# Performance work log

Hardware: AMD Instinct MI355X
Metric: run time of the kernel (lower is better)

The kernel has to match this reference:

```python
import jax, jax.numpy as jnp
import numpy as np

D_MODEL = 512
N = 1024
BS = 64


def setup_inputs() -> dict:
    key = jax.random.key(0)
    ks = jax.random.split(key, 4)
    x = jax.random.normal(ks[0], (BS, N, D_MODEL), dtype=jnp.float32)
    # nn.Linear init per init_weights(): weight ~ N(0, 0.001), bias = 0
    Wq = 0.001 * jax.random.normal(ks[1], (D_MODEL, D_MODEL), dtype=jnp.float32)
    Wk = 0.001 * jax.random.normal(ks[2], (D_MODEL, D_MODEL), dtype=jnp.float32)
    Wv = 0.001 * jax.random.normal(ks[3], (D_MODEL, D_MODEL), dtype=jnp.float32)
    bq = jnp.zeros((D_MODEL,), dtype=jnp.float32)
    bk = jnp.zeros((D_MODEL,), dtype=jnp.float32)
    bv = jnp.zeros((D_MODEL,), dtype=jnp.float32)
    pos_bias = jnp.ones((N, N), dtype=jnp.float32)  # nn.Parameter(ones)
    return {"x": x, "Wq": Wq, "bq": bq, "Wk": Wk, "bk": bk,
            "Wv": Wv, "bv": bv, "pos_bias": pos_bias}


def reference(x, Wq, bq, Wk, bk, Wv, bv, pos_bias):
    # q,k,v: [bs, n, d] via Linear (y = x W^T + b)
    q = jnp.einsum('bnd,ed->bne', x, Wq) + bq
    k = jnp.einsum('bnd,ed->bne', x, Wk) + bk
    v = jnp.einsum('bnd,ed->bne', x, Wv) + bv
    # exp(k[b,j,d] + bias[i,j]) factorizes exactly: exp(bias) * exp(k).
    # This avoids the (n, bs, n, d) broadcast intermediate of the original
    # while computing identical math.
    ek = jnp.exp(k)                                   # [bs, n, d]
    eb = jnp.exp(pos_bias)                            # [n_i, n_j]
    numerator = jnp.einsum('ij,bjd->bid', eb, ek * v)  # sum over j
    denominator = jnp.einsum('ij,bjd->bid', eb, ek)
    out = jax.nn.sigmoid(q) * (numerator / denominator)  # [bs, n, d]
    return out
```

## Files before the change

kernel.cpp:

```cpp
#include <hip/hip_runtime.h>
#include <hip/hip_bf16.h>
#include <stdint.h>


#define NSEQ 1024
#define DM   512

typedef __attribute__((ext_vector_type(8))) short bf16x8;
typedef __attribute__((ext_vector_type(4))) float f32x4;

static __device__ __forceinline__ float b2f(unsigned short u) {
    union { uint32_t i; float f; } c; c.i = ((uint32_t)u) << 16; return c.f;
}
static __device__ __forceinline__ unsigned short f2b(float f) {
    union { float f; uint32_t i; } c; c.f = f;
    uint32_t r = c.i + 0x7FFFu + ((c.i >> 16) & 1u);
    return (unsigned short)(r >> 16);
}
static __device__ __forceinline__ void gl_lds16(const unsigned short* g, unsigned short* l) {
    __builtin_amdgcn_global_load_lds(
        (const __attribute__((address_space(1))) unsigned int*)(g),
        (__attribute__((address_space(3))) unsigned int*)(l), 16, 0, 0);
}

#define PH_BAR() do { asm volatile("" ::: "memory"); \
    __builtin_amdgcn_s_barrier(); asm volatile("" ::: "memory"); } while (0)

__global__ void k_flag0(unsigned int* flag) { *flag = 0u; }

__global__ void k_flag(const float* __restrict__ pb, unsigned int* __restrict__ flag) {
    int i = blockIdx.x * 256 + threadIdx.x;
    float4 v = reinterpret_cast<const float4*>(pb)[i];
    float p0 = pb[0];
    if (v.x != p0 || v.y != p0 || v.z != p0 || v.w != p0) atomicOr(flag, 1u);
}

__global__ void k_eb(const float* __restrict__ pb, unsigned short* __restrict__ eb,
                     const unsigned int* __restrict__ flag) {
    if (*flag == 0u) return;
    int i = blockIdx.x * 256 + threadIdx.x;
    float4 v = reinterpret_cast<const float4*>(pb)[i];
    union { unsigned short u[4]; uint2 p; } o;
    o.u[0] = f2b(__expf(v.x)); o.u[1] = f2b(__expf(v.y));
    o.u[2] = f2b(__expf(v.z)); o.u[3] = f2b(__expf(v.w));
    reinterpret_cast<uint2*>(eb)[i] = o.p;
}

__global__ void k_cvt(const float* __restrict__ src, unsigned short* __restrict__ dst) {
    int i = blockIdx.x * 256 + threadIdx.x;
    const float4* p = reinterpret_cast<const float4*>(src) + (size_t)i * 2;
    float4 f0 = p[0], f1 = p[1];
    union { unsigned short u[8]; int4 v; } o;
    o.u[0]=f2b(f0.x); o.u[1]=f2b(f0.y); o.u[2]=f2b(f0.z); o.u[3]=f2b(f0.w);
    o.u[4]=f2b(f1.x); o.u[5]=f2b(f1.y); o.u[6]=f2b(f1.z); o.u[7]=f2b(f1.w);
    reinterpret_cast<int4*>(dst)[i] = o.v;
}

__global__ void k_cvt_kv(const float* __restrict__ src, unsigned short* __restrict__ Wb,
                         int toff) {
    int i = blockIdx.x * 256 + threadIdx.x;
    int r = i >> 6, c8 = i & 63;
    const float4* p = reinterpret_cast<const float4*>(src + (size_t)r * DM + c8 * 8);
    float4 f0 = p[0], f1 = p[1];
    union { unsigned short u[8]; int4 v; } o;
    o.u[0]=f2b(f0.x); o.u[1]=f2b(f0.y); o.u[2]=f2b(f0.z); o.u[3]=f2b(f0.w);
    o.u[4]=f2b(f1.x); o.u[5]=f2b(f1.y); o.u[6]=f2b(f1.z); o.u[7]=f2b(f1.w);
    int r2 = 512 + ((r >> 7) << 8) + ((r & 127) << 1) + toff;
    *reinterpret_cast<int4*>(&Wb[(size_t)r2 * DM + c8 * 8]) = o.v;
}

__launch_bounds__(512)
__global__ void k_kv(const float* __restrict__ x,
                     const unsigned short* __restrict__ Wb,
                     const float* __restrict__ bk, const float* __restrict__ bv,
                     unsigned short* __restrict__ Z,
                     float* __restrict__ P,
                     const unsigned int* __restrict__ flag)
{
    extern __shared__ unsigned short smem[];
    const int bid = blockIdx.x;
    const int logical = (bid & 7) * 128 + (bid >> 3);
    const int mtile = logical >> 2, e4 = logical & 3;
    const int brow = mtile * 256;
    const int b = brow >> 10, jtile = (brow >> 8) & 3;
    const bool uni = (*flag == 0u);

    const int tid = threadIdx.x;
    const int lane = tid & 63, wave = tid >> 6;
    const int wr = wave >> 2, wq = wave & 3;
    const int lrow = lane & 15, lkg = lane >> 4;
    const int po = lane >> 3, sub0 = (lane >> 2) & 1, qp = lane & 3;

    const float* Ax = x + (size_t)brow * DM;
    const unsigned short* Bb = Wb + (size_t)(512 + e4 * 256) * DM;

    f32x4 acc[8][4];
    const f32x4 z4 = {0.f, 0.f, 0.f, 0.f};
    #pragma unroll
    for (int a = 0; a < 8; ++a)
        #pragma unroll
        for (int c = 0; c < 4; ++c) acc[a][c] = z4;

    auto stgB = [&](int s, int h, int t) {
        int p = h * 64 + wave * 8 + po;
        int r = p * 2 + sub0;
        int col = (t << 5) + ((qp ^ (p & 3)) << 3);
        gl_lds16(Bb + (size_t)r * DM + col,
                 smem + 16384 + s * 8192 + (h * 64 + wave * 8) * 64);
    };
    auto ldAreg = [&](int t, int h, float4* f) {
        int p = h * 64 + wave * 8 + po;
        int r = p * 2 + sub0;
        int col = (t << 5) + ((qp ^ (p & 3)) << 3);
        const float4* sp = reinterpret_cast<const float4*>(Ax + (size_t)r * DM + col);
        f[0] = sp[0]; f[1] = sp[1];
    };
    auto wrA = [&](int s, int h, const float4* f) {
        union { unsigned short u[8]; int4 v; } o;
        o.u[0]=f2b(f[0].x); o.u[1]=f2b(f[0].y); o.u[2]=f2b(f[0].z); o.u[3]=f2b(f[0].w);
        o.u[4]=f2b(f[1].x); o.u[5]=f2b(f[1].y); o.u[6]=f2b(f[1].z); o.u[7]=f2b(f[1].w);
        *reinterpret_cast<int4*>(
            smem + s * 8192 + (h * 64 + wave * 8) * 64 + lane * 8) = o.v;
    };
    auto ldAf = [&](int s, int h, bf16x8* af) {
        const unsigned short* base = smem + s * 8192;
        #pragma unroll
        for (int mi = 0; mi < 4; ++mi) {
            int r = wr * 128 + h * 64 + mi * 16 + lrow, p = r >> 1;
            af[mi] = *reinterpret_cast<const bf16x8*>(
                base + p * 64 + (r & 1) * 32 + ((lkg ^ (p & 3)) << 3));
        }
    };
    auto ldBf = [&](int s, bf16x8* bf) {
        const unsigned short* base = smem + 16384 + s * 8192;
        #pragma unroll
        for (int ni = 0; ni < 4; ++ni) {
            int r = wq * 64 + ni * 16 + lrow, p = r >> 1;
            bf[ni] = *reinterpret_cast<const bf16x8*>(
                base + p * 64 + (r & 1) * 32 + ((lkg ^ (p & 3)) << 3));
        }
    };
    auto mfma16 = [&](int h, bf16x8* af, bf16x8* bf) {
        __builtin_amdgcn_s_setprio(1);
        #pragma unroll
        for (int mi = 0; mi < 4; ++mi)
            #pragma unroll
            for (int ni = 0; ni < 4; ++ni)
                acc[h * 4 + mi][ni] = __builtin_amdgcn_mfma_f32_16x16x32_bf16(
                    af[mi], bf[ni], acc[h * 4 + mi][ni], 0, 0, 0);
        __builtin_amdgcn_s_setprio(0);
    };

    {
        float4 fA0[2], fA1[2];
        ldAreg(0, 0, fA0); ldAreg(0, 1, fA1);
        stgB(0, 0, 0); stgB(0, 1, 0);
        wrA(0, 0, fA0); wrA(0, 1, fA1);
        __syncthreads();
    }
    #pragma unroll 1
    for (int t = 0; t < 16; ++t) {
        const int s = t & 1, sn = s ^ 1;
        const bool more = (t + 1 < 16);
        float4 fN0[2], fN1[2];
        if (more) {
            ldAreg(t + 1, 0, fN0); ldAreg(t + 1, 1, fN1);
            stgB(sn, 0, t + 1); stgB(sn, 1, t + 1);
        }
        bf16x8 af[4], bfr[4];
        ldBf(s, bfr); ldAf(s, 0, af);
        mfma16(0, af, bfr);
        ldAf(s, 1, af);
        mfma16(1, af, bfr);
        if (more) { wrA(sn, 0, fN0); wrA(sn, 1, fN1); }
        __syncthreads();
    }

    if (uni) {
        const int sub = lane & 1;
        float* SF = reinterpret_cast<float*>(smem);
        float se[4], sv2[4];
        #pragma unroll
        for (int ni = 0; ni < 4; ++ni) {
            int n = wq * 64 + ni * 16 + lrow;
            int d = e4 * 128 + (n >> 1);
            float bia = sub ? bv[d] : bk[d];
            float accv = 0.f, acce = 0.f;
            #pragma unroll
            for (int mi = 0; mi < 8; ++mi) {
                #pragma unroll
                for (int r = 0; r < 4; ++r) {
                    float val = acc[mi][ni][r] + bia;
                    float e = sub ? val : __expf(val);
                    float partner = __shfl_xor(e, 1);
                    if (!sub) { accv += e * partner; acce += e; }
                }
            }
            accv += __shfl_xor(accv, 16); accv += __shfl_xor(accv, 32);
            acce += __shfl_xor(acce, 16); acce += __shfl_xor(acce, 32);
            se[ni] = acce; sv2[ni] = accv;
        }
        __syncthreads();
        if (sub == 0 && lkg == 0) {
            #pragma unroll
            for (int ni = 0; ni < 4; ++ni) {
                int dl = wq * 32 + ni * 8 + (lrow >> 1);
                SF[wr * 256 + dl * 2]     = sv2[ni];
                SF[wr * 256 + dl * 2 + 1] = se[ni];
            }
        }
        __syncthreads();
        if (tid < 128) {
            int dl = tid, d = e4 * 128 + dl;
            float num = SF[dl * 2]     + SF[256 + dl * 2];
            float den = SF[dl * 2 + 1] + SF[256 + dl * 2 + 1];
            P[b * 2048 + jtile * 512 + d] = num;
            P[131072 + b * 2048 + jtile * 512 + d] = den;
        }
    } else {
        unsigned short* T = smem;
        #pragma unroll
        for (int pp = 0; pp < 2; ++pp) {
            __syncthreads();
            if (wr == pp) {
                #pragma unroll
                for (int mi = 0; mi < 8; ++mi) {
                    int m0 = mi*16 + lkg*4;
                    #pragma unroll
                    for (int ni = 0; ni < 4; ++ni) {
                        int n = wq*64 + ni*16 + lrow;
                        int sub = n & 1;
                        int d = e4 * 128 + (n >> 1);
                        float bia = sub ? bv[d] : bk[d];
                        union { unsigned short u[4]; uint2 p; } o;
                        #pragma unroll
                        for (int r = 0; r < 4; ++r) {
                            float tv = acc[mi][ni][r] + bia;
                            o.u[r] = f2b(sub ? tv : __expf(tv));
                        }
                        *reinterpret_cast<uint2*>(&T[n * 136 + m0]) = o.p;
                    }
                }
            }
            __syncthreads();
            const int j0 = (brow & (NSEQ - 1)) + pp * 128;
            #pragma unroll
            for (int it = 0; it < 8; ++it) {
                int idx = it * 512 + tid;
                int zr = idx >> 4, jg = idx & 15;
                int t = zr >> 7, dli = zr & 127;
                int d = e4 * 128 + dli;
                union { unsigned short u[8]; int4 v; } o;
                if (t == 0) {
                    union { unsigned short u[8]; int4 v; } pe, pv;
                    pe.v = *reinterpret_cast<const int4*>(&T[(2*dli)     * 136 + jg*8]);
                    pv.v = *reinterpret_cast<const int4*>(&T[(2*dli + 1) * 136 + jg*8]);
                    #pragma unroll
                    for (int j = 0; j < 8; ++j) o.u[j] = f2b(b2f(pe.u[j]) * b2f(pv.u[j]));
                } else {
                    o.v = *reinterpret_cast<const int4*>(&T[(2*dli) * 136 + jg*8]);
                }
                int nz = ((d >> 4) << 5) + t * 16 + (d & 15);
                size_t off = ((size_t)(b * NSEQ + nz)) * NSEQ + j0 + jg * 8;
                *reinterpret_cast<int4*>(&Z[off]) = o.v;
            }
        }
    }
}

__launch_bounds__(256)
__global__ void k_sum2(const float* __restrict__ P,
                       const unsigned int* __restrict__ flag,
                       float* __restrict__ R)
{
    if (*flag != 0u) return;
    int gid = blockIdx.x * 256 + threadIdx.x;
    int b = gid >> 9, d = gid & 511;
    const float* p0 = P + b * 2048 + d;
    const float* p1 = P + 131072 + b * 2048 + d;
    float num = p0[0] + p0[512] + p0[1024] + p0[1536];
    float den = p1[0] + p1[512] + p1[1024] + p1[1536];
    R[gid] = num / den;
}

__launch_bounds__(512)
__global__ void k_q(const float* __restrict__ x,
                    const unsigned short* __restrict__ Wb,
                    const float* __restrict__ bq,
                    const float* __restrict__ R,
                    unsigned short* __restrict__ s_out,
                    float* __restrict__ out,
                    const unsigned int* __restrict__ flag)
{
    extern __shared__ unsigned short smem[];
    const int bid = blockIdx.x;
    const int logical = (bid & 7) * 256 + (bid >> 3);
    const int mtile = logical >> 2, etile = logical & 3;
    const int brow = mtile * 128;
    const int ecol = etile * 128;
    const int b = brow >> 10;
    const bool uni = (*flag == 0u);

    const int tid = threadIdx.x;
    const int lane = tid & 63, wave = tid >> 6;
    const int wr = wave >> 2, wq = wave & 3;
    const int lrow = lane & 15, lkg = lane >> 4;
    const int po = lane >> 3, sub0 = (lane >> 2) & 1, qp = lane & 3;

    const float* Ax = x + (size_t)brow * DM;
    const unsigned short* Bb = Wb + (size_t)ecol * DM;

    f32x4 acc[4][2];
    const f32x4 z4 = {0.f, 0.f, 0.f, 0.f};
    #pragma unroll
    for (int a = 0; a < 4; ++a)
        #pragma unroll
        for (int c = 0; c < 2; ++c) acc[a][c] = z4;

    auto stgB = [&](int s, int t) {
        int p = wave * 8 + po;
        int r = p * 2 + sub0;
        int col = (t << 5) + ((qp ^ (p & 3)) << 3);
        gl_lds16(Bb + (size_t)r * DM + col,
                 smem + 8192 + s * 4096 + (wave * 8) * 64);
    };
    auto ldAreg = [&](int t, float4* f) {
        int p = wave * 8 + po;
        int r = p * 2 + sub0;
        int col = (t << 5) + ((qp ^ (p & 3)) << 3);
        const float4* sp = reinterpret_cast<const float4*>(Ax + (size_t)r * DM + col);
        f[0] = sp[0]; f[1] = sp[1];
    };
    auto wrA = [&](int s, const float4* f) {
        union { unsigned short u[8]; int4 v; } o;
        o.u[0]=f2b(f[0].x); o.u[1]=f2b(f[0].y); o.u[2]=f2b(f[0].z); o.u[3]=f2b(f[0].w);
        o.u[4]=f2b(f[1].x); o.u[5]=f2b(f[1].y); o.u[6]=f2b(f[1].z); o.u[7]=f2b(f[1].w);
        *reinterpret_cast<int4*>(
            smem + s * 4096 + (wave * 8) * 64 + lane * 8) = o.v;
    };
    auto ldAf = [&](int s, bf16x8* af) {
        const unsigned short* base = smem + s * 4096;
        #pragma unroll
        for (int mi = 0; mi < 4; ++mi) {
            int r = wr * 64 + mi * 16 + lrow, p = r >> 1;
            af[mi] = *reinterpret_cast<const bf16x8*>(
                base + p * 64 + (r & 1) * 32 + ((lkg ^ (p & 3)) << 3));
        }
    };
    auto ldBf = [&](int s, bf16x8* bf) {
        const unsigned short* base = smem + 8192 + s * 4096;
        #pragma unroll
        for (int ni = 0; ni < 2; ++ni) {
            int r = wq * 32 + ni * 16 + lrow, p = r >> 1;
            bf[ni] = *reinterpret_cast<const bf16x8*>(
                base + p * 64 + (r & 1) * 32 + ((lkg ^ (p & 3)) << 3));
        }
    };

    {
        float4 fA[2];
        ldAreg(0, fA);
        stgB(0, 0);
        wrA(0, fA);
        __syncthreads();
    }
    #pragma unroll 1
    for (int t = 0; t < 16; ++t) {
        const int s = t & 1, sn = s ^ 1;
        const bool more = (t + 1 < 16);
        float4 fN[2];
        if (more) { ldAreg(t + 1, fN); stgB(sn, t + 1); }
        bf16x8 af[4], bf[2];
        ldBf(s, bf); ldAf(s, af);
        __builtin_amdgcn_s_setprio(1);
        #pragma unroll
        for (int mi = 0; mi < 4; ++mi)
            #pragma unroll
            for (int ni = 0; ni < 2; ++ni)
                acc[mi][ni] = __builtin_amdgcn_mfma_f32_16x16x32_bf16(
                    af[mi], bf[ni], acc[mi][ni], 0, 0, 0);
        __builtin_amdgcn_s_setprio(0);
        if (more) wrA(sn, fN);
        __syncthreads();
    }

    unsigned short* T = smem;
    #pragma unroll
    for (int mi = 0; mi < 4; ++mi) {
        int m0 = wr * 64 + mi * 16 + lkg * 4;
        #pragma unroll
        for (int ni = 0; ni < 2; ++ni) {
            int nl = wq * 32 + ni * 16 + lrow;
            float bia = bq[ecol + nl];
            #pragma unroll
            for (int r = 0; r < 4; ++r) {
                float tq = acc[mi][ni][r] + bia;
                float sg = __builtin_amdgcn_rcpf(1.f + __expf(-tq));
                T[(m0 + r) * 136 + nl] = f2b(sg);
            }
        }
    }
    __syncthreads();
    if (uni) {
        #pragma unroll
        for (int it = 0; it < 4; ++it) {
            int idx = it * 512 + tid;
            int m = idx >> 4, ng = idx & 15;
            union { unsigned short u[8]; int4 v; } sv;
            sv.v = *reinterpret_cast<const int4*>(&T[m * 136 + ng * 8]);
            int dcol = ecol + ng * 8;
            const float4* rp = reinterpret_cast<const float4*>(&R[b * 512 + dcol]);
            float4 r0 = rp[0], r1 = rp[1];
            float4 o0, o1;
            o0.x = b2f(sv.u[0]) * r0.x; o0.y = b2f(sv.u[1]) * r0.y;
            o0.z = b2f(sv.u[2]) * r0.z; o0.w = b2f(sv.u[3]) * r0.w;
            o1.x = b2f(sv.u[4]) * r1.x; o1.y = b2f(sv.u[5]) * r1.y;
            o1.z = b2f(sv.u[6]) * r1.z; o1.w = b2f(sv.u[7]) * r1.w;
            float4* op = reinterpret_cast<float4*>(&out[(size_t)(brow + m) * DM + dcol]);
            op[0] = o0; op[1] = o1;
        }
    } else {
        #pragma unroll
        for (int it = 0; it < 4; ++it) {
            int idx = it * 512 + tid;
            int m = idx >> 4, ng = idx & 15;
            int4 vv = *reinterpret_cast<const int4*>(&T[m * 136 + ng * 8]);
            *reinterpret_cast<int4*>(
                &s_out[(size_t)(brow + m) * DM + ecol + ng * 8]) = vv;
        }
    }
}

__launch_bounds__(512)
__global__ void k_aft(const unsigned short* __restrict__ eb,
                      const unsigned short* __restrict__ Z,
                      const unsigned short* __restrict__ s_in,
                      const unsigned int* __restrict__ flag,
                      float* __restrict__ out)
{
    if (*flag == 0u) return;
    extern __shared__ unsigned short smem[];
    const int bid = blockIdx.x;
    const int logical = (bid & 7) * 32 + (bid >> 3);
    const int itile = logical & 3, ncol = logical >> 2;
    const int i0 = itile * 256;

    const int tid = threadIdx.x;
    const int lane = tid & 63, wave = tid >> 6;
    const int wr = wave >> 2, wq = wave & 3;
    const int lrow = lane & 15, lkg = lane >> 4;
    const int po = lane >> 3, sub = (lane >> 2) & 1, qp = lane & 3;
    const int ch0 = wave * 2;

    const unsigned short* Abase = eb + (size_t)i0 * NSEQ;
    const unsigned short* Bbase = Z + (size_t)ncol * 4 * 256 * NSEQ;

    f32x4 acc[8][4];
    const f32x4 z4 = {0.f, 0.f, 0.f, 0.f};
    #pragma unroll
    for (int a = 0; a < 8; ++a)
        #pragma unroll
        for (int c = 0; c < 4; ++c) acc[a][c] = z4;

    auto half = [&](int isB, int d, int c) -> unsigned short* {
        return smem + isB * 32768 + (d * 2 + c) * 8192;
    };
    auto stg = [&](int isB, int d, int c, int t) {
        int ta = t & 63, gp = ta >> 4, tk = ta & 15;
        unsigned short* dst = half(isB, d, c);
        #pragma unroll
        for (int q2 = 0; q2 < 2; ++q2) {
            int ch = ch0 + q2;
            int p = ch * 8 + po, r = p * 2 + sub;
            int col = (tk << 6) + (c << 5) + ((qp ^ (p & 3)) << 3);
            const unsigned short* g = isB
                ? Bbase + ((size_t)(gp * 256 + r)) * NSEQ + col
                : Abase + (size_t)r * NSEQ + col;
            gl_lds16(g, dst + ch * 512);
        }
    };
    auto ldA = [&](int d, int c, int h, bf16x8* af) {
        const unsigned short* base = half(0, d, c);
        #pragma unroll
        for (int mi = 0; mi < 4; ++mi) {
            int r = wr * 128 + h * 64 + mi * 16 + lrow, p = r >> 1;
            af[mi] = *reinterpret_cast<const bf16x8*>(
                base + p * 64 + (r & 1) * 32 + ((lkg ^ (p & 3)) << 3));
        }
    };
    auto ldB = [&](int d, int c, bf16x8* bf) {
        const unsigned short* base = half(1, d, c);
        #pragma unroll
        for (int ni = 0; ni < 4; ++ni) {
            int r = wq * 64 + ni * 16 + lrow, p = r >> 1;
            bf[ni] = *reinterpret_cast<const bf16x8*>(
                base + p * 64 + (r & 1) * 32 + ((lkg ^ (p & 3)) << 3));
        }
    };
    auto mm = [&](int h, bf16x8* af, bf16x8* bf) {
        __builtin_amdgcn_s_setprio(1);
        #pragma unroll
        for (int mi = 0; mi < 4; ++mi)
            #pragma unroll
            for (int ni = 0; ni < 4; ++ni)
                acc[h * 4 + mi][ni] = __builtin_amdgcn_mfma_f32_16x16x32_bf16(
                    af[mi], bf[ni], acc[h * 4 + mi][ni], 0, 0, 0);
        __builtin_amdgcn_s_setprio(0);
    };

    stg(0, 0, 0, 0); stg(1, 0, 0, 0);
    stg(0, 0, 1, 0); stg(1, 0, 1, 0);
    stg(0, 1, 0, 1); stg(1, 1, 0, 1);
    asm volatile("s_waitcnt vmcnt(4)" ::: "memory");
    __builtin_amdgcn_s_barrier();
    asm volatile("" ::: "memory");

    #pragma unroll 1
    for (int g = 0; g < 4; ++g) {
        #pragma unroll 1
        for (int ii = 0; ii < 8; ++ii) {
            const int T = (g << 4) + (ii << 1);
            const int U = T + 1, T2 = T + 2, U2 = T + 3;
            bf16x8 af[4], bf[4];
            ldB(0, 0, bf); ldA(0, 0, 0, af); stg(0, 1, 1, U);
            PH_BAR(); mm(0, af, bf); PH_BAR();
            ldA(0, 0, 1, af); stg(1, 1, 1, U);
            PH_BAR(); mm(1, af, bf); PH_BAR();
            ldB(0, 1, bf); ldA(0, 1, 0, af); stg(0, 0, 0, T2);
            PH_BAR(); mm(0, af, bf); PH_BAR();
            ldA(0, 1, 1, af); stg(1, 0, 0, T2);
            asm volatile("s_waitcnt vmcnt(4)" ::: "memory");
            PH_BAR(); mm(1, af, bf); PH_BAR();
            ldB(1, 0, bf); ldA(1, 0, 0, af); stg(0, 0, 1, T2);
            PH_BAR(); mm(0, af, bf); PH_BAR();
            ldA(1, 0, 1, af); stg(1, 0, 1, T2);
            PH_BAR(); mm(1, af, bf); PH_BAR();
            ldB(1, 1, bf); ldA(1, 1, 0, af); stg(0, 1, 0, U2);
            PH_BAR(); mm(0, af, bf); PH_BAR();
            ldA(1, 1, 1, af); stg(1, 1, 0, U2);
            asm volatile("s_waitcnt vmcnt(4)" ::: "memory");
            PH_BAR(); mm(1, af, bf); PH_BAR();
        }
        const int n0 = (ncol * 4 + g) * 256;
        #pragma unroll
        for (int mi = 0; mi < 8; ++mi) {
            int i = i0 + wr*128 + mi*16 + lkg*4;
            #pragma unroll
            for (int pi = 0; pi < 2; ++pi) {
                int nA = n0 + wq*64 + pi*32 + lrow;
                int b  = nA >> 10, nn = nA & (NSEQ - 1);
                int d  = ((nn >> 5) << 4) + (nn & 15);
                #pragma unroll
                for (int r = 0; r < 4; ++r) {
                    size_t o = ((size_t)(b * NSEQ + i + r)) * DM + d;
                    out[o] = b2f(s_in[o]) * acc[mi][pi*2][r] / acc[mi][pi*2 + 1][r];
                }
                acc[mi][pi*2] = z4; acc[mi][pi*2 + 1] = z4;
            }
        }
    }
    asm volatile("s_waitcnt vmcnt(0)" ::: "memory");
}

extern "C" void kernel_launch(void* const* d_in, const int* in_sizes, int n_in,
                              void* d_out, int out_size, void* d_ws, size_t ws_size,
                              hipStream_t stream)
{
    const float* x  = (const float*)d_in[0];
    const float* Wq = (const float*)d_in[1];
    const float* bq = (const float*)d_in[2];
    const float* Wk = (const float*)d_in[3];
    const float* bk = (const float*)d_in[4];
    const float* Wv = (const float*)d_in[5];
    const float* bv = (const float*)d_in[6];
    const float* pb = (const float*)d_in[7];
    float* out = (float*)d_out;

    char* ws = (char*)d_ws;
    unsigned short* eb   = (unsigned short*)(ws);
    float*          Pbuf = (float*)(ws);
    unsigned short* Wb   = (unsigned short*)(ws + ((size_t)2 << 20));
    unsigned int*   flag = (unsigned int*)(ws + 0x380000);
    float*          Rbuf = (float*)(ws + 0x384000);
    unsigned short* s    = (unsigned short*)(ws + ((size_t)68  << 20));
    unsigned short* Z    = (unsigned short*)(ws + ((size_t)132 << 20));

    k_flag0<<<1, 1, 0, stream>>>(flag);
    k_flag<<<1024, 256, 0, stream>>>(pb, flag);
    k_eb <<<1024, 256, 0, stream>>>(pb, eb, flag);
    k_cvt<<<128,   256, 0, stream>>>(Wq, Wb);
    k_cvt_kv<<<128, 256, 0, stream>>>(Wk, Wb, 0);
    k_cvt_kv<<<128, 256, 0, stream>>>(Wv, Wb, 1);
    k_kv<<<1024, 512, 69632, stream>>>(x, Wb, bk, bv, Z, Pbuf, flag);
    k_sum2<<<128, 256, 0, stream>>>(Pbuf, flag, Rbuf);
    k_q<<<2048, 512, 34816, stream>>>(x, Wb, bq, Rbuf, s, out, flag);
    k_aft<<<256, 512, 131072, stream>>>(eb, Z, s, flag, out);
}
```

Measured before the change: 189.8 us.

## Deepen A-operand register prefetch to two tiles with explicit waitcnt barriers

Restructures the K-loops of both the KV and Q projection GEMM kernels so the fp32 A tile is loaded into registers two iterations ahead, using ping-pong register sets and a 2x manually unrolled loop. Replaces __syncthreads with explicit s_waitcnt vmcnt(N) plus s_barrier, so outstanding global loads for the following tile can stay in flight across the barrier. Tile indices are masked with &15, so the loop issues harmless redundant loads past the end instead of branching. This hides global-load latency at the cost of more registers, extra wasted loads at the tail, and reliance on a hand-counted vmcnt.

```diff
diff --git a/kernel.cpp b/kernel.cpp
--- a/kernel.cpp
+++ b/kernel.cpp
@@ -104,14 +104,14 @@
     auto stgB = [&](int s, int h, int t) {
         int p = h * 64 + wave * 8 + po;
         int r = p * 2 + sub0;
-        int col = (t << 5) + ((qp ^ (p & 3)) << 3);
+        int col = ((t & 15) << 5) + ((qp ^ (p & 3)) << 3);
         gl_lds16(Bb + (size_t)r * DM + col,
                  smem + 16384 + s * 8192 + (h * 64 + wave * 8) * 64);
     };
     auto ldAreg = [&](int t, int h, float4* f) {
         int p = h * 64 + wave * 8 + po;
         int r = p * 2 + sub0;
-        int col = (t << 5) + ((qp ^ (p & 3)) << 3);
+        int col = ((t & 15) << 5) + ((qp ^ (p & 3)) << 3);
         const float4* sp = reinterpret_cast<const float4*>(Ax + (size_t)r * DM + col);
         f[0] = sp[0]; f[1] = sp[1];
     };
@@ -151,30 +151,37 @@
         __builtin_amdgcn_s_setprio(0);
     };
 
-    {
-        float4 fA0[2], fA1[2];
-        ldAreg(0, 0, fA0); ldAreg(0, 1, fA1);
-        stgB(0, 0, 0); stgB(0, 1, 0);
-        wrA(0, 0, fA0); wrA(0, 1, fA1);
-        __syncthreads();
-    }
+    float4 rE0[2], rE1[2], rO0[2], rO1[2];
+
+    ldAreg(0, 0, rE0); ldAreg(0, 1, rE1);
+    stgB(0, 0, 0); stgB(0, 1, 0);
+    wrA(0, 0, rE0); wrA(0, 1, rE1);
+    ldAreg(1, 0, rO0); ldAreg(1, 1, rO1);
+    asm volatile("s_waitcnt vmcnt(4) lgkmcnt(0)" ::: "memory");
+    __builtin_amdgcn_s_barrier();
+
+    #define KV_TILE(t, s, sn, c0, c1, n0q, n1q)                              \
+    {                                                                         \
+        stgB(sn, 0, (t) + 1); stgB(sn, 1, (t) + 1);                           \
+        ldAreg((t) + 2, 0, n0q); ldAreg((t) + 2, 1, n1q);                     \
+        bf16x8 af[4], bfr[4];                                                 \
+        ldBf(s, bfr); ldAf(s, 0, af);                                         \
+        mfma16(0, af, bfr);                                                   \
+        ldAf(s, 1, af);                                                       \
+        mfma16(1, af, bfr);                                                   \
+        wrA(sn, 0, c0); wrA(sn, 1, c1);    \
+        asm volatile("s_waitcnt vmcnt(4) lgkmcnt(0)" ::: "memory");           \
+        __builtin_amdgcn_s_barrier();                                         \
+    }
+
     #pragma unroll 1
-    for (int t = 0; t < 16; ++t) {
-        const int s = t & 1, sn = s ^ 1;
-        const bool more = (t + 1 < 16);
-        float4 fN0[2], fN1[2];
-        if (more) {
-            ldAreg(t + 1, 0, fN0); ldAreg(t + 1, 1, fN1);
-            stgB(sn, 0, t + 1); stgB(sn, 1, t + 1);
-        }
-        bf16x8 af[4], bfr[4];
-        ldBf(s, bfr); ldAf(s, 0, af);
-        mfma16(0, af, bfr);
-        ldAf(s, 1, af);
-        mfma16(1, af, bfr);
-        if (more) { wrA(sn, 0, fN0); wrA(sn, 1, fN1); }
-        __syncthreads();
-    }
+    for (int tt = 0; tt < 16; tt += 2) {
+        KV_TILE(tt,     tt & 1, (tt & 1) ^ 1, rO0, rO1, rE0, rE1);
+        KV_TILE(tt + 1, (tt + 1) & 1, tt & 1, rE0, rE1, rO0, rO1);
+    }
+    #undef KV_TILE
+    asm volatile("s_waitcnt vmcnt(0) lgkmcnt(0)" ::: "memory");
+    __builtin_amdgcn_s_barrier();
 
     if (uni) {
         const int sub = lane & 1;
@@ -320,14 +327,14 @@
     auto stgB = [&](int s, int t) {
         int p = wave * 8 + po;
         int r = p * 2 + sub0;
-        int col = (t << 5) + ((qp ^ (p & 3)) << 3);
+        int col = ((t & 15) << 5) + ((qp ^ (p & 3)) << 3);
         gl_lds16(Bb + (size_t)r * DM + col,
                  smem + 8192 + s * 4096 + (wave * 8) * 64);
     };
     auto ldAreg = [&](int t, float4* f) {
         int p = wave * 8 + po;
         int r = p * 2 + sub0;
-        int col = (t << 5) + ((qp ^ (p & 3)) << 3);
+        int col = ((t & 15) << 5) + ((qp ^ (p & 3)) << 3);
         const float4* sp = reinterpret_cast<const float4*>(Ax + (size_t)r * DM + col);
         f[0] = sp[0]; f[1] = sp[1];
     };
@@ -357,32 +364,41 @@
         }
     };
 
-    {
-        float4 fA[2];
-        ldAreg(0, fA);
-        stgB(0, 0);
-        wrA(0, fA);
-        __syncthreads();
-    }
+    float4 rE[2], rO[2];
+    ldAreg(0, rE);
+    stgB(0, 0);
+    wrA(0, rE);
+    ldAreg(1, rO);
+    asm volatile("s_waitcnt vmcnt(2) lgkmcnt(0)" ::: "memory");
+    __builtin_amdgcn_s_barrier();
+
+    #define Q_TILE(t, s, sn, cur, nxt)                                        \
+    {                                                                         \
+        stgB(sn, (t) + 1);                                                    \
+        ldAreg((t) + 2, nxt);                                                 \
+        bf16x8 af[4], bf[2];                                                  \
+        ldBf(s, bf); ldAf(s, af);                                             \
+        __builtin_amdgcn_s_setprio(1);                                        \
+        _Pragma("unroll")                                                     \
+        for (int mi = 0; mi < 4; ++mi)                                        \
+            _Pragma("unroll")                                                 \
+            for (int ni = 0; ni < 2; ++ni)                                    \
+                acc[mi][ni] = __builtin_amdgcn_mfma_f32_16x16x32_bf16(        \
+                    af[mi], bf[ni], acc[mi][ni], 0, 0, 0);                    \
+        __builtin_amdgcn_s_setprio(0);                                        \
+        wrA(sn, cur);                                                         \
+        asm volatile("s_waitcnt vmcnt(2) lgkmcnt(0)" ::: "memory");           \
+        __builtin_amdgcn_s_barrier();                                         \
+    }
+
     #pragma unroll 1
-    for (int t = 0; t < 16; ++t) {
-        const int s = t & 1, sn = s ^ 1;
-        const bool more = (t + 1 < 16);
-        float4 fN[2];
-        if (more) { ldAreg(t + 1, fN); stgB(sn, t + 1); }
-        bf16x8 af[4], bf[2];
-        ldBf(s, bf); ldAf(s, af);
-        __builtin_amdgcn_s_setprio(1);
-        #pragma unroll
-        for (int mi = 0; mi < 4; ++mi)
-            #pragma unroll
-            for (int ni = 0; ni < 2; ++ni)
-                acc[mi][ni] = __builtin_amdgcn_mfma_f32_16x16x32_bf16(
-                    af[mi], bf[ni], acc[mi][ni], 0, 0, 0);
-        __builtin_amdgcn_s_setprio(0);
-        if (more) wrA(sn, fN);
-        __syncthreads();
-    }
+    for (int tt = 0; tt < 16; tt += 2) {
+        Q_TILE(tt,     tt & 1, (tt & 1) ^ 1, rO, rE);
+        Q_TILE(tt + 1, (tt + 1) & 1, tt & 1, rE, rO);
+    }
+    #undef Q_TILE
+    asm volatile("s_waitcnt vmcnt(0) lgkmcnt(0)" ::: "memory");
+    __builtin_amdgcn_s_barrier();
 
     unsigned short* T = smem;
     #pragma unroll
```

Measured after the change: 204.2 us. 7.6% more time.
